# Optimization experiments

Measured on AMD Instinct MI355X. Metric: run time of the kernel, lower is better.

The kernel has to match this reference:

```python
import jax, jax.numpy as jnp
import numpy as np

B, S, D_IN = 4, 2048, 1024
EMBED, HEADS = 1024, 16
HEAD_DIM = EMBED // HEADS


def setup_inputs() -> dict:
    key = jax.random.key(0)
    k1, k2, k3 = jax.random.split(key, 3)
    x = jax.random.normal(k1, (B, S, D_IN), dtype=jnp.float32)
    # xavier-uniform-ish init scales
    lim_qkv = float(np.sqrt(6.0 / (D_IN + 3 * EMBED)))
    lim_o = float(np.sqrt(6.0 / (EMBED + EMBED)))
    w_qkv = jax.random.uniform(k2, (3 * EMBED, D_IN), minval=-lim_qkv, maxval=lim_qkv, dtype=jnp.float32)
    b_qkv = jnp.zeros((3 * EMBED,), dtype=jnp.float32)
    w_o = jax.random.uniform(k3, (EMBED, EMBED), minval=-lim_o, maxval=lim_o, dtype=jnp.float32)
    b_o = jnp.zeros((EMBED,), dtype=jnp.float32)
    return {"x": x, "w_qkv": w_qkv, "b_qkv": b_qkv, "w_o": w_o, "b_o": b_o}


def reference(x, w_qkv, b_qkv, w_o, b_o):
    b, s, _ = x.shape
    qkv = jnp.einsum('bsi,oi->bso', x, w_qkv) + b_qkv            # (b, s, 3E)
    qkv = qkv.reshape(b, s, HEADS, 3 * HEAD_DIM).transpose(0, 2, 1, 3)  # (b, h, s, 3d)
    q, k, v = jnp.split(qkv, 3, axis=-1)                          # each (b, h, s, d)
    scale = 1.0 / jnp.sqrt(jnp.float32(HEAD_DIM))
    attn = jnp.einsum('bhqd,bhkd->bhqk', q, k) * scale            # (b, h, s, s)
    attn = jax.nn.softmax(attn, axis=-1)
    vals = jnp.einsum('bhqk,bhkd->bhqd', attn, v)                 # (b, h, s, d)
    # NOTE: original torch code reshapes (b,h,s,d) -> (b,s,e) WITHOUT transposing
    # heads back; jnp.reshape reproduces that flattening exactly.
    vals = vals.reshape(b, s, EMBED)
    out = jnp.einsum('bse,oe->bso', vals, w_o) + b_o              # (b, s, E)
    return out
```

## Files before the change

kernel.cpp:

```cpp
#include <hip/hip_runtime.h>
#include <stdint.h>
#include <stddef.h>

#define DEVINL __device__ __forceinline__

typedef unsigned short u16;
typedef unsigned int u32;
typedef __attribute__((ext_vector_type(8))) short short8;
typedef __attribute__((ext_vector_type(4))) float f32x4;
typedef __attribute__((ext_vector_type(4))) u32 u32x4;
typedef __attribute__((ext_vector_type(2))) u32 u32x2;

#define QSCALE 0.18033688011112042f

DEVINL u16 f2bf(float f) {
    u32 u = __builtin_bit_cast(u32, f);
    u32 r = (u + 0x7fffu + ((u >> 16) & 1u)) >> 16;
    return (u16)r;
}

DEVINL void gld_lds16(const void* g, void* l) {
    __builtin_amdgcn_global_load_lds(
        (__attribute__((address_space(1))) u32*)(uintptr_t)g,
        (__attribute__((address_space(3))) u32*)l, 16, 0, 0);
}

DEVINL u32 pack_bf16_trunc(float lo, float hi) {
    return __builtin_amdgcn_perm(__builtin_bit_cast(u32, hi),
                                 __builtin_bit_cast(u32, lo), 0x07060302u);
}

__global__ void prep_inputs(const float* __restrict__ x, const float* __restrict__ wqkv,
                            const float* __restrict__ bqkv, const float* __restrict__ wo,
                            u16* __restrict__ xb, u16* __restrict__ wqb,
                            u16* __restrict__ wob, float* __restrict__ bsc) {
    int blk = blockIdx.x;
    if (blk < 6144) {
        const float* src; u16* dst; int base; bool qscale = false;
        if (blk < 4096)      { src = x;    dst = xb;  base = blk; }
        else if (blk < 5632) { src = wqkv; dst = wqb; base = blk - 4096; qscale = true; }
        else                 { src = wo;   dst = wob; base = blk - 5632; }
        int i = (base * 256 + threadIdx.x) * 8;
        float sc = 1.0f;
        if (qscale) { int row = i >> 10; if ((row % 192) < 64) sc = QSCALE; }
        float4 a = *(const float4*)(src + i);
        float4 c = *(const float4*)(src + i + 4);
        union { u16 s[8]; u32x4 v; } t;
        t.s[0] = f2bf(a.x * sc); t.s[1] = f2bf(a.y * sc); t.s[2] = f2bf(a.z * sc); t.s[3] = f2bf(a.w * sc);
        t.s[4] = f2bf(c.x * sc); t.s[5] = f2bf(c.y * sc); t.s[6] = f2bf(c.z * sc); t.s[7] = f2bf(c.w * sc);
        *(u32x4*)(dst + i) = t.v;
    } else {
        int i = (blk - 6144) * 256 + threadIdx.x;
        float sc = ((i % 192) < 64) ? QSCALE : 1.0f;
        bsc[i] = bqkv[i] * sc;
    }
}

__global__ void gemm_qkv(const u16* __restrict__ A, const u16* __restrict__ Bm,
                         const float* __restrict__ bias, u16* __restrict__ qkvb,
                         u16* __restrict__ vtb) {
    const int K = 1024, N = 3072;
    __shared__ u16 As[128 * 32];
    __shared__ u16 Bs[128 * 32];
    const int tid = threadIdx.x;
    const int lane = tid & 63;
    const int wv = tid >> 6, wr = wv >> 1, wc = wv & 1;
    const int l15 = lane & 15, quad = lane >> 4;
    const int m0 = blockIdx.y * 128, n0 = blockIdx.x * 128;

    f32x4 acc[4][4];
#pragma unroll
    for (int i = 0; i < 4; i++)
#pragma unroll
        for (int j = 0; j < 4; j++) acc[i][j] = (f32x4){0.f, 0.f, 0.f, 0.f};

    const u16* Ab = A + (size_t)m0 * K;
    const u16* Bb = Bm + (size_t)n0 * K;
    const int srow = tid >> 2;
    const int sc8 = (tid & 3) * 8;

    for (int k0 = 0; k0 < K; k0 += 32) {
#pragma unroll
        for (int i = 0; i < 2; i++) {
            int row = i * 64 + srow;
            gld_lds16(Ab + (size_t)row * K + k0 + sc8, (char*)As + (size_t)(i * 256 + tid) * 16);
            gld_lds16(Bb + (size_t)row * K + k0 + sc8, (char*)Bs + (size_t)(i * 256 + tid) * 16);
        }
        __syncthreads();
        short8 af[4], bf8[4];
#pragma unroll
        for (int mi = 0; mi < 4; mi++)
            af[mi] = *(const short8*)(As + (wr * 64 + mi * 16 + l15) * 32 + quad * 8);
#pragma unroll
        for (int ni = 0; ni < 4; ni++)
            bf8[ni] = *(const short8*)(Bs + (wc * 64 + ni * 16 + l15) * 32 + quad * 8);
#pragma unroll
        for (int mi = 0; mi < 4; mi++)
#pragma unroll
            for (int ni = 0; ni < 4; ni++)
                acc[mi][ni] = __builtin_amdgcn_mfma_f32_16x16x32_bf16(af[mi], bf8[ni], acc[mi][ni], 0, 0, 0);
        __syncthreads();
    }

#pragma unroll
    for (int mi = 0; mi < 4; mi++) {
        int row_b = m0 + wr * 64 + mi * 16 + quad * 4;
#pragma unroll
        for (int ni = 0; ni < 4; ni++) {
            int c0 = n0 + wc * 64 + ni * 16;
            int sec0 = c0 % 192;
            float bv = bias[c0 + l15];
            float v0 = acc[mi][ni][0] + bv;
            float v1 = acc[mi][ni][1] + bv;
            float v2 = acc[mi][ni][2] + bv;
            float v3 = acc[mi][ni][3] + bv;
            if (sec0 >= 128) {
                int hh = c0 / 192;
                int b = row_b >> 11;
                int s = row_b & 2047;
                int d = sec0 - 128 + l15;
                u32 lo = (u32)f2bf(v0) | ((u32)f2bf(v1) << 16);
                u32 hi = (u32)f2bf(v2) | ((u32)f2bf(v3) << 16);
                *(u32x2*)(vtb + ((size_t)((b * 16 + hh) * 64 + d)) * 2048 + s) = (u32x2){lo, hi};
            } else {
                int col = c0 + l15;
                qkvb[(size_t)(row_b + 0) * N + col] = f2bf(v0);
                qkvb[(size_t)(row_b + 1) * N + col] = f2bf(v1);
                qkvb[(size_t)(row_b + 2) * N + col] = f2bf(v2);
                qkvb[(size_t)(row_b + 3) * N + col] = f2bf(v3);
            }
        }
    }
}

__global__ void gemm_out(const u16* __restrict__ A, const u16* __restrict__ Bm,
                         const float* __restrict__ bias, float* __restrict__ C) {
    const int K = 1024, N = 1024;
    __shared__ u16 As[128 * 32];
    __shared__ u16 Bs[64 * 32];
    const int tid = threadIdx.x;
    const int lane = tid & 63;
    const int wv = tid >> 6, wr = wv >> 1, wc = wv & 1;
    const int l15 = lane & 15, quad = lane >> 4;
    const int m0 = blockIdx.y * 128, n0 = blockIdx.x * 64;

    f32x4 acc[4][2];
#pragma unroll
    for (int i = 0; i < 4; i++)
#pragma unroll
        for (int j = 0; j < 2; j++) acc[i][j] = (f32x4){0.f, 0.f, 0.f, 0.f};

    const u16* Ab = A + (size_t)m0 * K;
    const u16* Bb = Bm + (size_t)n0 * K;
    const int srow = tid >> 2;
    const int sc8 = (tid & 3) * 8;

    for (int k0 = 0; k0 < K; k0 += 32) {
#pragma unroll
        for (int i = 0; i < 2; i++)
            gld_lds16(Ab + (size_t)(i * 64 + srow) * K + k0 + sc8, (char*)As + (size_t)(i * 256 + tid) * 16);
        gld_lds16(Bb + (size_t)srow * K + k0 + sc8, (char*)Bs + (size_t)tid * 16);
        __syncthreads();
        short8 af[4], bf8[2];
#pragma unroll
        for (int mi = 0; mi < 4; mi++)
            af[mi] = *(const short8*)(As + (wr * 64 + mi * 16 + l15) * 32 + quad * 8);
#pragma unroll
        for (int ni = 0; ni < 2; ni++)
            bf8[ni] = *(const short8*)(Bs + (wc * 32 + ni * 16 + l15) * 32 + quad * 8);
#pragma unroll
        for (int mi = 0; mi < 4; mi++)
#pragma unroll
            for (int ni = 0; ni < 2; ni++)
                acc[mi][ni] = __builtin_amdgcn_mfma_f32_16x16x32_bf16(af[mi], bf8[ni], acc[mi][ni], 0, 0, 0);
        __syncthreads();
    }

#pragma unroll
    for (int mi = 0; mi < 4; mi++) {
        int row_b = m0 + wr * 64 + mi * 16 + quad * 4;
#pragma unroll
        for (int ni = 0; ni < 2; ni++) {
            int col = n0 + wc * 32 + ni * 16 + l15;
            float bv = bias[col];
#pragma unroll
            for (int r = 0; r < 4; r++)
                C[(size_t)(row_b + r) * N + col] = acc[mi][ni][r] + bv;
        }
    }
}

__launch_bounds__(256, 4)
__global__ void flash_attn(const u16* __restrict__ qkv, const u16* __restrict__ vt,
                           u16* __restrict__ vals2) {
    __shared__ u16 Ks[64 * 64];
    __shared__ u16 Vts[64 * 64];
    __shared__ u16 Ps[4][32 * 64];

    const int tid = threadIdx.x;
    const int lane = tid & 63, wv = tid >> 6;
    const int l15 = lane & 15, quad = lane >> 4;
    const int e7 = (l15 & 7) * 8;
    const int s0 = blockIdx.x * 128;
    const int bh = blockIdx.y, b = bh >> 4, h = bh & 15;

    short8 qf[2][2];
    const u16* qbase = qkv + (size_t)(b * 2048 + s0 + wv * 32) * 3072 + h * 192;
#pragma unroll
    for (int qi = 0; qi < 2; qi++)
#pragma unroll
        for (int ks = 0; ks < 2; ks++)
            qf[qi][ks] = *(const short8*)(qbase + (size_t)(qi * 16 + l15) * 3072 + ks * 32 + quad * 8);

    f32x4 o_acc[2][4];
    f32x4 sum_acc[2];
#pragma unroll
    for (int qi = 0; qi < 2; qi++) {
        sum_acc[qi] = (f32x4){0.f, 0.f, 0.f, 0.f};
#pragma unroll
        for (int nd = 0; nd < 4; nd++) o_acc[qi][nd] = (f32x4){0.f, 0.f, 0.f, 0.f};
    }

    const u16* kg = qkv + (size_t)(b * 2048) * 3072 + h * 192 + 64;
    const u16* vg = vt + (size_t)bh * 64 * 2048;

    const int lrow = lane >> 3;
    const int lgr  = (lane & 7) ^ lrow;
    const int r0   = wv * 8 + lrow;

    const short8 ones = (short8){0x3F80, 0x3F80, 0x3F80, 0x3F80, 0x3F80, 0x3F80, 0x3F80, 0x3F80};

    for (int kb = 0; kb < 2048; kb += 64) {
        __syncthreads();
#pragma unroll
        for (int j = 0; j < 2; j++) {
            int row = j * 32 + r0;
            gld_lds16(kg + (size_t)(kb + row) * 3072 + lgr * 8,
                      (char*)Ks + (size_t)(j * 256 + tid) * 16);
            gld_lds16(vg + (size_t)row * 2048 + kb + lgr * 8,
                      (char*)Vts + (size_t)(j * 256 + tid) * 16);
        }
        __syncthreads();

        f32x4 s_acc[4][2];
#pragma unroll
        for (int ki = 0; ki < 4; ki++)
#pragma unroll
            for (int qi = 0; qi < 2; qi++) s_acc[ki][qi] = (f32x4){0.f, 0.f, 0.f, 0.f};
#pragma unroll
        for (int ki = 0; ki < 4; ki++) {
#pragma unroll
            for (int ks = 0; ks < 2; ks++) {
                short8 kf = *(const short8*)(Ks + (ki * 16 + l15) * 64 + ((ks * 32 + quad * 8) ^ e7));
#pragma unroll
                for (int qi = 0; qi < 2; qi++)
                    s_acc[ki][qi] = __builtin_amdgcn_mfma_f32_16x16x32_bf16(kf, qf[qi][ks], s_acc[ki][qi], 0, 0, 0);
            }
        }

#pragma unroll
        for (int ki = 0; ki < 4; ki++)
#pragma unroll
            for (int qi = 0; qi < 2; qi++) {
                float p0 = __builtin_amdgcn_exp2f(s_acc[ki][qi][0]);
                float p1 = __builtin_amdgcn_exp2f(s_acc[ki][qi][1]);
                float p2 = __builtin_amdgcn_exp2f(s_acc[ki][qi][2]);
                float p3 = __builtin_amdgcn_exp2f(s_acc[ki][qi][3]);
                u32x2 pk = (u32x2){pack_bf16_trunc(p0, p1), pack_bf16_trunc(p2, p3)};
                *(u32x2*)(Ps[wv] + (qi * 16 + l15) * 64 + ((ki * 16 + quad * 4) ^ e7)) = pk;
            }

#pragma unroll
        for (int c = 0; c < 2; c++) {
            short8 ap[2];
#pragma unroll
            for (int qi = 0; qi < 2; qi++)
                ap[qi] = *(const short8*)(Ps[wv] + (qi * 16 + l15) * 64 + ((c * 32 + quad * 8) ^ e7));
#pragma unroll
            for (int qi = 0; qi < 2; qi++)
                sum_acc[qi] = __builtin_amdgcn_mfma_f32_16x16x32_bf16(ap[qi], ones, sum_acc[qi], 0, 0, 0);
#pragma unroll
            for (int nd = 0; nd < 4; nd++) {
                short8 bv = *(const short8*)(Vts + (nd * 16 + l15) * 64 + ((c * 32 + quad * 8) ^ e7));
#pragma unroll
                for (int qi = 0; qi < 2; qi++)
                    o_acc[qi][nd] = __builtin_amdgcn_mfma_f32_16x16x32_bf16(ap[qi], bv, o_acc[qi][nd], 0, 0, 0);
            }
        }
    }

#pragma unroll
    for (int qi = 0; qi < 2; qi++) {
        f32x4 inv;
#pragma unroll
        for (int r = 0; r < 4; r++) inv[r] = 1.0f / sum_acc[qi][r];
#pragma unroll
        for (int nd = 0; nd < 4; nd++) {
            int d = nd * 16 + l15;
#pragma unroll
            for (int r = 0; r < 4; r++) {
                int s = s0 + wv * 32 + qi * 16 + quad * 4 + r;
                size_t row2 = (size_t)(b * 2048 + h * 128 + (s >> 4));
                int col2 = ((s & 15) << 6) + d;
                vals2[row2 * 1024 + col2] = f2bf(o_acc[qi][nd][r] * inv[r]);
            }
        }
    }
}

extern "C" void kernel_launch(void* const* d_in, const int* in_sizes, int n_in,
                              void* d_out, int out_size, void* d_ws, size_t ws_size,
                              hipStream_t stream) {
    (void)in_sizes; (void)n_in; (void)out_size; (void)ws_size;
    const float* x      = (const float*)d_in[0];
    const float* w_qkv  = (const float*)d_in[1];
    const float* b_qkv  = (const float*)d_in[2];
    const float* w_o    = (const float*)d_in[3];
    const float* b_o    = (const float*)d_in[4];
    float* out = (float*)d_out;

    char* ws = (char*)d_ws;
    u16* xb   = (u16*)(ws);
    u16* wqb  = (u16*)(ws + 16777216);
    u16* wob  = (u16*)(ws + 23068672);
    u16* qkvb = (u16*)(ws + 25165824);
    u16* vtb  = (u16*)(ws + 75497472);
    u16* v2b  = (u16*)(ws + 92274688);
    float* bsc = (float*)(ws + 92274688);

    prep_inputs<<<6156, 256, 0, stream>>>(x, w_qkv, b_qkv, w_o, xb, wqb, wob, bsc);

    gemm_qkv<<<dim3(24, 64), 256, 0, stream>>>(xb, wqb, bsc, qkvb, vtb);

    flash_attn<<<dim3(16, 64), 256, 0, stream>>>(qkvb, vtb, v2b);

    gemm_out<<<dim3(16, 64), 256, 0, stream>>>(v2b, wob, b_o, out);
}
```

Before: 269.7 us.

## Double-buffer K/V tiles and keep softmax probabilities in registers via permlane swaps

K and V^T tiles are double-buffered in LDS so the next tile's async global-to-LDS load is issued before computing on the current one, removing one barrier per iteration. The exponentiated scores are packed to bf16 and rearranged into the MFMA A-operand layout using v_permlane32/16_swap instead of writing and re-reading them through a per-wave LDS buffer. This cuts LDS traffic and latency but depends on the permlane shuffle producing exactly the k-ordering the V operand expects.

Result: no change. 272.2 us (+0.9%).

```diff
diff --git a/kernel.cpp b/kernel.cpp
--- a/kernel.cpp
+++ b/kernel.cpp
@@ -28,6 +28,23 @@
 DEVINL u32 pack_bf16_trunc(float lo, float hi) {
     return __builtin_amdgcn_perm(__builtin_bit_cast(u32, hi),
                                  __builtin_bit_cast(u32, lo), 0x07060302u);
+}
+
+DEVINL void plswap32(u32 &a, u32 &b) {
+#if __has_builtin(__builtin_amdgcn_permlane32_swap)
+    u32x2 r = __builtin_amdgcn_permlane32_swap(a, b, false, false);
+    a = r[0]; b = r[1];
+#else
+    asm("v_permlane32_swap_b32 %0, %1" : "+v"(a), "+v"(b));
+#endif
+}
+DEVINL void plswap16(u32 &a, u32 &b) {
+#if __has_builtin(__builtin_amdgcn_permlane16_swap)
+    u32x2 r = __builtin_amdgcn_permlane16_swap(a, b, false, false);
+    a = r[0]; b = r[1];
+#else
+    asm("v_permlane16_swap_b32 %0, %1" : "+v"(a), "+v"(b));
+#endif
 }
 
 __global__ void prep_inputs(const float* __restrict__ x, const float* __restrict__ wqkv,
@@ -193,9 +210,8 @@
 __launch_bounds__(256, 4)
 __global__ void flash_attn(const u16* __restrict__ qkv, const u16* __restrict__ vt,
                            u16* __restrict__ vals2) {
-    __shared__ u16 Ks[64 * 64];
-    __shared__ u16 Vts[64 * 64];
-    __shared__ u16 Ps[4][32 * 64];
+    __shared__ u16 Ks[2][64 * 64];
+    __shared__ u16 Vts[2][64 * 64];
 
     const int tid = threadIdx.x;
     const int lane = tid & 63, wv = tid >> 6;
@@ -230,17 +246,27 @@
 
     const short8 ones = (short8){0x3F80, 0x3F80, 0x3F80, 0x3F80, 0x3F80, 0x3F80, 0x3F80, 0x3F80};
 
+#pragma unroll
+    for (int j = 0; j < 2; j++) {
+        int row = j * 32 + r0;
+        gld_lds16(kg + (size_t)row * 3072 + lgr * 8, (char*)&Ks[0][0] + (size_t)(j * 256 + tid) * 16);
+        gld_lds16(vg + (size_t)row * 2048 + lgr * 8, (char*)&Vts[0][0] + (size_t)(j * 256 + tid) * 16);
+    }
+    __syncthreads();
+
+    int cur = 0;
     for (int kb = 0; kb < 2048; kb += 64) {
-        __syncthreads();
-#pragma unroll
-        for (int j = 0; j < 2; j++) {
-            int row = j * 32 + r0;
-            gld_lds16(kg + (size_t)(kb + row) * 3072 + lgr * 8,
-                      (char*)Ks + (size_t)(j * 256 + tid) * 16);
-            gld_lds16(vg + (size_t)row * 2048 + kb + lgr * 8,
-                      (char*)Vts + (size_t)(j * 256 + tid) * 16);
-        }
-        __syncthreads();
+        if (kb + 64 < 2048) {
+            int nb = cur ^ 1;
+#pragma unroll
+            for (int j = 0; j < 2; j++) {
+                int row = j * 32 + r0;
+                gld_lds16(kg + (size_t)(kb + 64 + row) * 3072 + lgr * 8,
+                          (char*)&Ks[nb][0] + (size_t)(j * 256 + tid) * 16);
+                gld_lds16(vg + (size_t)row * 2048 + kb + 64 + lgr * 8,
+                          (char*)&Vts[nb][0] + (size_t)(j * 256 + tid) * 16);
+            }
+        }
 
         f32x4 s_acc[4][2];
 #pragma unroll
@@ -251,42 +277,50 @@
         for (int ki = 0; ki < 4; ki++) {
 #pragma unroll
             for (int ks = 0; ks < 2; ks++) {
-                short8 kf = *(const short8*)(Ks + (ki * 16 + l15) * 64 + ((ks * 32 + quad * 8) ^ e7));
+                short8 kf = *(const short8*)(&Ks[cur][0] + (ki * 16 + l15) * 64 + ((ks * 32 + quad * 8) ^ e7));
 #pragma unroll
                 for (int qi = 0; qi < 2; qi++)
                     s_acc[ki][qi] = __builtin_amdgcn_mfma_f32_16x16x32_bf16(kf, qf[qi][ks], s_acc[ki][qi], 0, 0, 0);
             }
         }
 
-#pragma unroll
-        for (int ki = 0; ki < 4; ki++)
+        short8 ap[2][2];
+#pragma unroll
+        for (int c = 0; c < 2; c++)
 #pragma unroll
             for (int qi = 0; qi < 2; qi++) {
-                float p0 = __builtin_amdgcn_exp2f(s_acc[ki][qi][0]);
-                float p1 = __builtin_amdgcn_exp2f(s_acc[ki][qi][1]);
-                float p2 = __builtin_amdgcn_exp2f(s_acc[ki][qi][2]);
-                float p3 = __builtin_amdgcn_exp2f(s_acc[ki][qi][3]);
-                u32x2 pk = (u32x2){pack_bf16_trunc(p0, p1), pack_bf16_trunc(p2, p3)};
-                *(u32x2*)(Ps[wv] + (qi * 16 + l15) * 64 + ((ki * 16 + quad * 4) ^ e7)) = pk;
+                u32 w0 = pack_bf16_trunc(__builtin_amdgcn_exp2f(s_acc[2 * c][qi][0]),
+                                         __builtin_amdgcn_exp2f(s_acc[2 * c][qi][1]));
+                u32 w1 = pack_bf16_trunc(__builtin_amdgcn_exp2f(s_acc[2 * c][qi][2]),
+                                         __builtin_amdgcn_exp2f(s_acc[2 * c][qi][3]));
+                u32 w2 = pack_bf16_trunc(__builtin_amdgcn_exp2f(s_acc[2 * c + 1][qi][0]),
+                                         __builtin_amdgcn_exp2f(s_acc[2 * c + 1][qi][1]));
+                u32 w3 = pack_bf16_trunc(__builtin_amdgcn_exp2f(s_acc[2 * c + 1][qi][2]),
+                                         __builtin_amdgcn_exp2f(s_acc[2 * c + 1][qi][3]));
+                plswap32(w0, w2);
+                plswap32(w1, w3);
+                plswap16(w0, w2);
+                plswap16(w1, w3);
+                u32x4 wf = (u32x4){w0, w1, w2, w3};
+                ap[qi][c] = __builtin_bit_cast(short8, wf);
             }
 
 #pragma unroll
         for (int c = 0; c < 2; c++) {
-            short8 ap[2];
 #pragma unroll
             for (int qi = 0; qi < 2; qi++)
-                ap[qi] = *(const short8*)(Ps[wv] + (qi * 16 + l15) * 64 + ((c * 32 + quad * 8) ^ e7));
-#pragma unroll
-            for (int qi = 0; qi < 2; qi++)
-                sum_acc[qi] = __builtin_amdgcn_mfma_f32_16x16x32_bf16(ap[qi], ones, sum_acc[qi], 0, 0, 0);
+                sum_acc[qi] = __builtin_amdgcn_mfma_f32_16x16x32_bf16(ap[qi][c], ones, sum_acc[qi], 0, 0, 0);
 #pragma unroll
             for (int nd = 0; nd < 4; nd++) {
-                short8 bv = *(const short8*)(Vts + (nd * 16 + l15) * 64 + ((c * 32 + quad * 8) ^ e7));
+                short8 bv = *(const short8*)(&Vts[cur][0] + (nd * 16 + l15) * 64 + ((c * 32 + quad * 8) ^ e7));
 #pragma unroll
                 for (int qi = 0; qi < 2; qi++)
-                    o_acc[qi][nd] = __builtin_amdgcn_mfma_f32_16x16x32_bf16(ap[qi], bv, o_acc[qi][nd], 0, 0, 0);
-            }
-        }
+                    o_acc[qi][nd] = __builtin_amdgcn_mfma_f32_16x16x32_bf16(ap[qi][c], bv, o_acc[qi][nd], 0, 0, 0);
+            }
+        }
+
+        __syncthreads();
+        cur ^= 1;
     }
 
 #pragma unroll
```
